# Kernel tuning notes

Measured on AMD Instinct MI355X. Metric: run time of the kernel, lower is better.

## Reference

```python
import jax, jax.numpy as jnp
import numpy as np

B, L, E, H = 1024, 18, 300, 300
VW, VS = 100000, 2186


def setup_inputs() -> dict:
    key = jax.random.key(0)
    ks = jax.random.split(key, 16)
    word = jax.random.randint(ks[0], (B, 1), 0, VW)
    sememes = jax.random.randint(ks[1], (B, L), 0, VS)
    word_table = jax.random.normal(ks[2], (VW, E), jnp.float32) * 0.1
    sem_table = jax.random.normal(ks[3], (VS, E), jnp.float32) * 0.1
    sem_table = sem_table.at[0].set(0.0)  # padding_idx=0 -> zero row
    s = 1.0 / np.sqrt(H)

    def u(k, shape):
        return jax.random.uniform(k, shape, jnp.float32, -s, s)

    return {
        "word": word, "sememes": sememes,
        "word_table": word_table, "sem_table": sem_table,
        "Wih_f": u(ks[4], (4 * H, 2 * E)), "Whh_f": u(ks[5], (4 * H, H)),
        "bih_f": u(ks[6], (4 * H,)), "bhh_f": u(ks[7], (4 * H,)),
        "Wih_b": u(ks[8], (4 * H, 2 * E)), "Whh_b": u(ks[9], (4 * H, H)),
        "bih_b": u(ks[10], (4 * H,)), "bhh_b": u(ks[11], (4 * H,)),
        "Wa": u(ks[12], (H, 2 * H)), "ba": jnp.zeros((H,), jnp.float32),
        "Wb": u(ks[13], (E, E)), "bb": jnp.zeros((E,), jnp.float32),
    }


def _lstm(x, Wih, Whh, bih, bhh, reverse):
    # x: [B, L, 2E]; PyTorch gate order i, f, g, o
    xg = jnp.einsum('ble,ge->blg', x, Wih) + bih + bhh  # [B, L, 4H]
    Hh = Whh.shape[1]
    Bn = x.shape[0]

    def step(carry, xt):
        h, c = carry
        g = xt + h @ Whh.T
        i, f, gg, o = jnp.split(g, 4, axis=-1)
        i = jax.nn.sigmoid(i)
        f = jax.nn.sigmoid(f)
        gg = jnp.tanh(gg)
        o = jax.nn.sigmoid(o)
        c = f * c + i * gg
        h = o * jnp.tanh(c)
        return (h, c), h

    init = (jnp.zeros((Bn, Hh), x.dtype), jnp.zeros((Bn, Hh), x.dtype))
    _, hs = jax.lax.scan(step, init, jnp.swapaxes(xg, 0, 1), reverse=reverse)
    return jnp.swapaxes(hs, 0, 1)  # [B, L, H]


def reference(word, sememes, word_table, sem_table,
              Wih_f, Whh_f, bih_f, bhh_f,
              Wih_b, Whh_b, bih_b, bhh_b,
              Wa, ba, Wb, bb):
    w = word_table[word[:, 0]]      # [B, E]
    s = sem_table[sememes]          # [B, L, E]
    # AvgPool2d((18,1)) over the L=18 axis (zeros included in the mean)
    a_g = jnp.mean(s, axis=1)       # [B, E]
    v_g = jax.nn.relu(a_g @ Wb.T + bb)  # dropout is identity at inference
    # Vectorized replacement of the per-element python loop:
    # padding slot (index 0 -> zero embedding) gets cat(sem, sem) = zeros,
    # otherwise cat(word_emb, sem).
    mask = (sememes == 0)[..., None]                    # [B, L, 1]
    first = jnp.where(mask, s, w[:, None, :])           # [B, L, E]
    x = jnp.concatenate([first, s], axis=-1)            # [B, L, 2E]
    hf = _lstm(x, Wih_f, Whh_f, bih_f, bhh_f, reverse=False)
    hb = _lstm(x, Wih_b, Whh_b, bih_b, bhh_b, reverse=True)
    Vh = jnp.concatenate([hf, hb], axis=-1)             # [B, L, 2H]
    V = jax.nn.relu(jnp.einsum('blh,oh->blo', Vh, Wa) + ba)
    return V, v_g
```

## Files before the change

### kernel.cpp

```cpp
#include <hip/hip_runtime.h>
#include <cstddef>
#include <cstdint>
#include <math.h>

#define B_   1024
#define L_   18
#define E_   300
#define H_   300
#define M_   (B_*L_)
#define G4_  (4*H_)
#define K2E_ (2*E_)

#define NPAD 2432
#define PSTR 2432
#define M2P  2304

#define OFF_P1   ((size_t)0)
#define OFF_P2   (OFF_P1 + (size_t)1024*PSTR)
#define OFF_HCAT (OFF_P2 + (size_t)M2P*PSTR)
#define OFF_AG   (OFF_HCAT + (size_t)M_*608/2)
#define OFF_WBT  (OFF_AG  + (size_t)B_*E_)
#define OFF_WFF  (OFF_WBT + 90000)
#define OFF_WFB  (OFF_WFF + 194560)
#define OFF_WAT  (OFF_WFB + 194560)
#define OFF_WCP  (OFF_WAT + 92416)
#define OFF_HP   (OFF_WCP + 778240)
#define OFF_C    (OFF_HP + 655360)

#define HPSTR 327680

#define VOFF ((size_t)M_*H_)

typedef short bf16x8 __attribute__((ext_vector_type(8)));
typedef float f32x4  __attribute__((ext_vector_type(4)));

__device__ __forceinline__ short f2bf(float f) {
    union { float f; uint32_t u; } c; c.f = f;
    uint32_t u = c.u + 0x7fffu + ((c.u >> 16) & 1u);
    return (short)(u >> 16);
}

__global__ void k_prep(const float* __restrict__ Wb, float* __restrict__ WbT)
{
    int idx = blockIdx.x * 256 + threadIdx.x;
    if (idx < 90000) {
        int o = idx % 300;
        int k = idx / 300;
        WbT[idx] = Wb[o * 300 + k];
    }
}

__global__ __launch_bounds__(256) void k_prep_wcp(const float* __restrict__ Wih_f,
                                                  const float* __restrict__ Wih_b,
                                                  short* __restrict__ WcatP)
{
    int idx = blockIdx.x * 256 + threadIdx.x;
    if (idx >= 2 * NPAD * 320) return;
    int p = idx / (NPAD * 320);
    int rem = idx - p * (NPAD * 320);
    int n = rem / 320;
    int kp = rem - n * 320;
    int fwd = (n < 1216);
    int nn = fwd ? n : n - 1216;
    float v = 0.f;
    if (kp < 300 && nn < G4_) {
        int u = nn >> 2, g = nn & 3;
        const float* W = fwd ? Wih_f : Wih_b;
        v = W[(size_t)(g * 300 + u) * K2E_ + (p ? 300 + kp : kp)];
    }
    WcatP[idx] = f2bf(v);
}

__global__ __launch_bounds__(256) void k_prep_whh(const float* __restrict__ Whh_f,
                                                  const float* __restrict__ Whh_b,
                                                  short* __restrict__ WFf,
                                                  short* __restrict__ WFb)
{
    int idx = blockIdx.x * 256 + threadIdx.x;
    if (idx >= 389120) return;
    int d = blockIdx.y;
    int chunk = idx >> 9;
    int rem   = idx & 511;
    int lane  = rem >> 3;
    int j     = rem & 7;
    int nt = chunk / 10, kt = chunk - nt * 10;
    int n = nt * 16 + (lane & 15);
    int k = kt * 32 + (lane >> 4) * 8 + j;
    float v = 0.f;
    if (n < G4_ && k < H_) {
        int u = n >> 2, g = n & 3;
        const float* W = d ? Whh_b : Whh_f;
        v = W[(size_t)(g * 300 + u) * H_ + k];
    }
    (d ? WFb : WFf)[idx] = f2bf(v);
}

__global__ __launch_bounds__(256) void k_prep_wa(const float* __restrict__ Wa,
                                                 short* __restrict__ WAT)
{
    int idx = blockIdx.x * 256 + threadIdx.x;
    if (idx >= 184832) return;
    int chunk = idx >> 9;
    int rem   = idx & 511;
    int lane  = rem >> 3;
    int j     = rem & 7;
    int nt = chunk / 19, kt = chunk - nt * 19;
    int o  = nt * 16 + (lane & 15);
    int kp = kt * 32 + (lane >> 4) * 8 + j;
    float v = 0.f;
    if (o < H_) {
        int k = -1;
        if (kp < 300)                   k = kp;
        else if (kp >= 304 && kp < 604) k = kp - 4;
        if (k >= 0) v = Wa[(size_t)o * K2E_ + k];
    }
    WAT[idx] = f2bf(v);
}

__global__ void k_zero(short* __restrict__ hcat, short* __restrict__ hp)
{
    int r = blockIdx.x * 256 + threadIdx.x;
    if (r < M_) {
        *(uint64_t*)&hcat[(size_t)r * 608 + 300] = 0ull;
        *(uint64_t*)&hcat[(size_t)r * 608 + 604] = 0ull;
    }
    uint64_t* hp8 = (uint64_t*)hp;
    for (int i = r; i < 327680; i += M_) hp8[i] = 0ull;
}

__global__ __launch_bounds__(256) void k_ag(const int* __restrict__ sem,
                                            const float* __restrict__ sem_table,
                                            float* __restrict__ ag)
{
    int b = blockIdx.x;
    __shared__ int sm[L_];
    if (threadIdx.x < L_) sm[threadIdx.x] = sem[b * L_ + threadIdx.x];
    __syncthreads();
    for (int e = threadIdx.x; e < E_; e += 256) {
        float s = 0.f;
        #pragma unroll
        for (int l = 0; l < L_; ++l) s += sem_table[sm[l] * E_ + e];
        ag[(size_t)b * E_ + e] = s * (1.0f / (float)L_);
    }
}

__global__ __launch_bounds__(256) void k_vg(const float* __restrict__ ag,
                                            const float* __restrict__ WbT,
                                            const float* __restrict__ bbv,
                                            float* __restrict__ out)
{
    int b0 = blockIdx.x * 16;
    __shared__ __align__(16) float ag_s[16 * E_];
    for (int idx = threadIdx.x; idx < 16 * E_; idx += 256)
        ag_s[idx] = ag[(size_t)b0 * E_ + idx];
    __syncthreads();
    for (int o = threadIdx.x; o < E_; o += 256) {
        float acc[16];
        #pragma unroll
        for (int i = 0; i < 16; ++i) acc[i] = 0.f;
        for (int k = 0; k < E_; ++k) {
            float w = WbT[k * E_ + o];
            #pragma unroll
            for (int i = 0; i < 16; ++i)
                acc[i] = fmaf(w, ag_s[i * E_ + k], acc[i]);
        }
        float bias = bbv[o];
        #pragma unroll
        for (int i = 0; i < 16; ++i) {
            float v = acc[i] + bias;
            out[VOFF + (size_t)(b0 + i) * E_ + o] = v > 0.f ? v : 0.f;
        }
    }
}

#define LDT 40

__global__ __launch_bounds__(256) void k_p(const int* __restrict__ word,
                                           const float* __restrict__ word_table,
                                           const float* __restrict__ sem_table,
                                           const short* __restrict__ WcatP,
                                           const float* __restrict__ bih_f,
                                           const float* __restrict__ bhh_f,
                                           const float* __restrict__ bih_b,
                                           const float* __restrict__ bhh_b,
                                           float* __restrict__ P1,
                                           float* __restrict__ P2)
{
    __shared__ __align__(16) short As[128 * LDT];
    __shared__ __align__(16) short Bs[128 * LDT];
    __shared__ const float* rowp[128];

    const int mb = blockIdx.x;
    const int p  = (mb >= 8);
    const int m0 = (p ? mb - 8 : mb) * 128;
    const int n0 = blockIdx.y * 128;
    const int tid = threadIdx.x;

    if (tid < 128) {
        int m = m0 + tid;
        rowp[tid] = p ? (m < 2186 ? sem_table + (size_t)m * E_ : (const float*)0)
                      : word_table + (size_t)word[m] * E_;
    }
    __syncthreads();

    f32x4 acc[4][4];
    #pragma unroll
    for (int i = 0; i < 4; ++i)
        #pragma unroll
        for (int j = 0; j < 4; ++j)
            acc[i][j] = (f32x4){0.f, 0.f, 0.f, 0.f};

    const int wv   = tid >> 6;
    const int lane = tid & 63;
    const int wm   = (wv >> 1) * 64;
    const int wn   = (wv & 1) * 64;
    const int lm   = lane & 15;
    const int quad = lane >> 4;

    const int r  = tid >> 1;
    const int kh = (tid & 1) * 16;
    const float* rp = rowp[r];
    const short* bsrc = WcatP + (size_t)p * (NPAD * 320) + (size_t)(n0 + r) * 320;

    for (int k0 = 0; k0 < 320; k0 += 32) {
        {
            const int kbase = k0 + kh;
            #pragma unroll
            for (int q = 0; q < 4; ++q) {
                int k = kbase + q * 4;
                float4 v = (k < E_ && rp) ? *(const float4*)&rp[k]
                                          : make_float4(0.f, 0.f, 0.f, 0.f);
                short4 s4;
                s4.x = f2bf(v.x); s4.y = f2bf(v.y);
                s4.z = f2bf(v.z); s4.w = f2bf(v.w);
                *(short4*)&As[r * LDT + kh + q * 4] = s4;
            }
        }
        {
            const short* src = bsrc + k0 + kh;
            *(int4*)&Bs[r * LDT + kh + 0] = *(const int4*)&src[0];
            *(int4*)&Bs[r * LDT + kh + 8] = *(const int4*)&src[8];
        }
        __syncthreads();

        bf16x8 af[4], bfr[4];
        #pragma unroll
        for (int i = 0; i < 4; ++i)
            af[i] = *(const bf16x8*)&As[(wm + 16 * i + lm) * LDT + quad * 8];
        #pragma unroll
        for (int j = 0; j < 4; ++j)
            bfr[j] = *(const bf16x8*)&Bs[(wn + 16 * j + lm) * LDT + quad * 8];
        #pragma unroll
        for (int i = 0; i < 4; ++i)
            #pragma unroll
            for (int j = 0; j < 4; ++j)
                acc[i][j] = __builtin_amdgcn_mfma_f32_16x16x32_bf16(
                    af[i], bfr[j], acc[i][j], 0, 0, 0);
        __syncthreads();
    }

    float* dst = p ? P2 : P1;
    #pragma unroll
    for (int j = 0; j < 4; ++j) {
        int n = n0 + wn + 16 * j + lm;
        float bias = 0.f;
        if (p) {
            int fwd = (n < 1216);
            int cc = fwd ? n : n - 1216;
            if (cc < G4_) {
                int u = cc >> 2, g = cc & 3;
                bias = fwd ? (bih_f[g * 300 + u] + bhh_f[g * 300 + u])
                           : (bih_b[g * 300 + u] + bhh_b[g * 300 + u]);
            }
        }
        #pragma unroll
        for (int i = 0; i < 4; ++i) {
            int mb2 = m0 + wm + 16 * i + quad * 4;
            #pragma unroll
            for (int reg = 0; reg < 4; ++reg)
                dst[(size_t)(mb2 + reg) * PSTR + n] = acc[i][j][reg] + bias;
        }
    }
}

__global__ __launch_bounds__(256) void k_step2(const float* __restrict__ P1,
                                               const float* __restrict__ P2,
                                               const int* __restrict__ sem,
                                               const short* __restrict__ WFf,
                                               const short* __restrict__ WFb,
                                               short* __restrict__ hp,
                                               float* __restrict__ cbuf,
                                               short* __restrict__ hcat,
                                               int s)
{
    const int d  = blockIdx.z;
    const short* WF = d ? WFb : WFf;
    const int t = d ? (L_ - 1 - s) : s;
    const short* hin = hp + (size_t)(d * 2 + ((s + 1) & 1)) * HPSTR;
    short*      hout = hp + (size_t)(d * 2 + (s & 1)) * HPSTR;
    short* hc = hcat + (d ? 304 : 0);
    float* cp = cbuf + (size_t)d * (1024 * 304);

    const int m0 = blockIdx.x * 64;
    const int rt0 = blockIdx.x * 4;
    const int nb = blockIdx.y;
    const int tid  = threadIdx.x;
    const int lane = tid & 63;
    const int wv   = tid >> 6;
    const int lm   = lane & 15;
    const int quad = lane >> 4;

    __shared__ __align__(16) float Cs[64][68];

    f32x4 acc[4];
    #pragma unroll
    for (int mt = 0; mt < 4; ++mt) acc[mt] = (f32x4){0.f, 0.f, 0.f, 0.f};

    if (s > 0) {
        const short* wp = WF + ((size_t)(nb * 4 + wv) * 10) * 512 + lane * 8;
        #pragma unroll
        for (int kt = 0; kt < 10; ++kt) {
            bf16x8 bf = *(const bf16x8*)(wp + kt * 512);
            #pragma unroll
            for (int mt = 0; mt < 4; ++mt) {
                bf16x8 af = *(const bf16x8*)&hin[((size_t)(rt0 + mt) * 10 + kt) * 512 + lane * 8];
                acc[mt] = __builtin_amdgcn_mfma_f32_16x16x32_bf16(af, bf, acc[mt], 0, 0, 0);
            }
        }
    }

    #pragma unroll
    for (int mt = 0; mt < 4; ++mt)
        #pragma unroll
        for (int r = 0; r < 4; ++r)
            Cs[mt * 16 + quad * 4 + r][wv * 16 + lm] = acc[mt][r];
    __syncthreads();

    const int m = tid >> 2;
    const int q = tid & 3;
    const int b = m0 + m;
    const int u0 = nb * 16 + 4 * q;
    if (u0 < H_) {
        const int svt = sem[b * L_ + t];
        const size_t pcol = (size_t)d * 1216 + 4 * u0;
        const float* p2r = P2 + (size_t)svt * PSTR + pcol;
        const float* p1r = P1 + (size_t)b * PSTR + pcol;
        float4 xv[4];
        #pragma unroll
        for (int i = 0; i < 4; ++i) xv[i] = *(const float4*)&p2r[4 * i];
        if (svt != 0) {
            #pragma unroll
            for (int i = 0; i < 4; ++i) {
                float4 a = *(const float4*)&p1r[4 * i];
                xv[i].x += a.x; xv[i].y += a.y; xv[i].z += a.z; xv[i].w += a.w;
            }
        }
        float4 cpv = (s > 0) ? *(const float4*)&cp[(size_t)b * 304 + u0]
                             : make_float4(0.f, 0.f, 0.f, 0.f);
        float cold[4] = {cpv.x, cpv.y, cpv.z, cpv.w};
        float cnew[4];
        short hn[4];
        #pragma unroll
        for (int i = 0; i < 4; ++i) {
            float4 gv = *(const float4*)&Cs[m][16 * q + 4 * i];
            float gi = xv[i].x + gv.x;
            float gf = xv[i].y + gv.y;
            float gg = xv[i].z + gv.z;
            float go = xv[i].w + gv.w;
            float iv = 1.f / (1.f + __expf(-gi));
            float fv = 1.f / (1.f + __expf(-gf));
            float tg = 1.f - 2.f / (__expf(2.f * gg) + 1.f);
            float ov = 1.f / (1.f + __expf(-go));
            float cc = fmaf(fv, cold[i], iv * tg);
            cnew[i] = cc;
            float th = 1.f - 2.f / (__expf(2.f * cc) + 1.f);
            hn[i] = f2bf(ov * th);
        }
        *(float4*)&cp[(size_t)b * 304 + u0] = make_float4(cnew[0], cnew[1], cnew[2], cnew[3]);
        short4 h4 = {hn[0], hn[1], hn[2], hn[3]};
        {
            int rt = b >> 4, ktu = u0 >> 5;
            int fl = (b & 15) | (((u0 >> 3) & 3) << 4);
            *(short4*)&hout[((size_t)(rt * 10 + ktu) * 512) + fl * 8 + (u0 & 7)] = h4;
        }
        *(short4*)&hc[((size_t)b * L_ + t) * 608 + u0] = h4;
    }
}

__global__ __launch_bounds__(256) void k_out(const short* __restrict__ hcat,
                                             const short* __restrict__ WAT,
                                             const float* __restrict__ ba,
                                             float* __restrict__ out)
{
    const int m0 = blockIdx.x * 64;
    const int tid = threadIdx.x;
    const int lane = tid & 63;
    const int wv = tid >> 6;
    const int lm = lane & 15;
    const int quad = lane >> 4;

    __shared__ __align__(16) short A_s[64][616];

    for (int idx = tid; idx < 4864; idx += 256) {
        int r = idx / 76, c8 = idx - r * 76;
        *(int4*)&A_s[r][c8 * 8] = *(const int4*)&hcat[(size_t)(m0 + r) * 608 + c8 * 8];
    }
    __syncthreads();

    f32x4 acc[4][5];
    #pragma unroll
    for (int mt = 0; mt < 4; ++mt)
        #pragma unroll
        for (int q = 0; q < 5; ++q)
            acc[mt][q] = (f32x4){0.f, 0.f, 0.f, 0.f};

    for (int kt = 0; kt < 19; ++kt) {
        bf16x8 af[4];
        #pragma unroll
        for (int mt = 0; mt < 4; ++mt)
            af[mt] = *(const bf16x8*)&A_s[mt * 16 + lm][kt * 32 + quad * 8];
        #pragma unroll
        for (int q = 0; q < 5; ++q) {
            int nt = wv + 4 * q;
            if (nt < 19) {
                bf16x8 bf = *(const bf16x8*)&WAT[((size_t)(nt * 19 + kt) * 64 + lane) * 8];
                #pragma unroll
                for (int mt = 0; mt < 4; ++mt)
                    acc[mt][q] = __builtin_amdgcn_mfma_f32_16x16x32_bf16(
                        af[mt], bf, acc[mt][q], 0, 0, 0);
            }
        }
    }

    #pragma unroll
    for (int q = 0; q < 5; ++q) {
        int nt = wv + 4 * q;
        if (nt < 19) {
            int o = nt * 16 + lm;
            if (o < H_) {
                float bias = ba[o];
                #pragma unroll
                for (int mt = 0; mt < 4; ++mt) {
                    #pragma unroll
                    for (int r = 0; r < 4; ++r) {
                        int m = m0 + mt * 16 + quad * 4 + r;
                        float v = acc[mt][q][r] + bias;
                        out[(size_t)m * H_ + o] = v > 0.f ? v : 0.f;
                    }
                }
            }
        }
    }
}

extern "C" void kernel_launch(void* const* d_in, const int* in_sizes, int n_in,
                              void* d_out, int out_size, void* d_ws, size_t ws_size,
                              hipStream_t stream) {
    const int*   word       = (const int*)  d_in[0];
    const int*   sem        = (const int*)  d_in[1];
    const float* word_table = (const float*)d_in[2];
    const float* sem_table  = (const float*)d_in[3];
    const float* Wih_f      = (const float*)d_in[4];
    const float* Whh_f      = (const float*)d_in[5];
    const float* bih_f      = (const float*)d_in[6];
    const float* bhh_f      = (const float*)d_in[7];
    const float* Wih_b      = (const float*)d_in[8];
    const float* Whh_b      = (const float*)d_in[9];
    const float* bih_b      = (const float*)d_in[10];
    const float* bhh_b      = (const float*)d_in[11];
    const float* Wa         = (const float*)d_in[12];
    const float* ba         = (const float*)d_in[13];
    const float* Wb         = (const float*)d_in[14];
    const float* bbv        = (const float*)d_in[15];

    float* out = (float*)d_out;
    float* ws  = (float*)d_ws;

    float* P1    = ws + OFF_P1;
    float* P2    = ws + OFF_P2;
    short* hcat  = (short*)(ws + OFF_HCAT);
    float* ag    = ws + OFF_AG;
    float* WbT   = ws + OFF_WBT;
    short* WFf   = (short*)(ws + OFF_WFF);
    short* WFb   = (short*)(ws + OFF_WFB);
    short* WAT   = (short*)(ws + OFF_WAT);
    short* WcatP = (short*)(ws + OFF_WCP);
    short* hp    = (short*)(ws + OFF_HP);
    float* cbuf  = ws + OFF_C;

    k_prep<<<dim3(352), dim3(256), 0, stream>>>(Wb, WbT);
    k_prep_wcp<<<dim3((2 * NPAD * 320 + 255) / 256), dim3(256), 0, stream>>>(
        Wih_f, Wih_b, WcatP);
    k_prep_whh<<<dim3(1520, 2), dim3(256), 0, stream>>>(Whh_f, Whh_b, WFf, WFb);
    k_prep_wa<<<dim3(722), dim3(256), 0, stream>>>(Wa, WAT);
    k_zero<<<dim3((M_ + 255) / 256), dim3(256), 0, stream>>>(hcat, hp);

    k_ag<<<dim3(B_), dim3(256), 0, stream>>>(sem, sem_table, ag);
    k_vg<<<dim3(B_ / 16), dim3(256), 0, stream>>>(ag, WbT, bbv, out);

    k_p<<<dim3(26, 19), dim3(256), 0, stream>>>(
        word, word_table, sem_table, WcatP,
        bih_f, bhh_f, bih_b, bhh_b, P1, P2);

    for (int s = 0; s < L_; ++s) {
        k_step2<<<dim3(16, 19, 2), dim3(256), 0, stream>>>(
            P1, P2, sem, WFf, WFb, hp, cbuf, hcat, s);
    }

    k_out<<<dim3(M_ / 64), dim3(256), 0, stream>>>(hcat, WAT, ba, out);
}
```

Baseline: 533.2 us.

## Fuse LSTM recurrence into one persistent cooperative kernel with grid sync

The 18 per-timestep k_step2 launches are replaced by one cooperative kernel, k_rec2, that loops over all timesteps and uses a grid-wide sync between steps. Each block keeps its slice of the recurrent weights and its cell state in registers and handles 128 rows instead of 64, which removes per-step launch overhead and repeated weight and cell-state traffic. In exchange, grid syncs and heavier register use per block limit it to 2 blocks per CU, and the old per-step path stays as a fallback when cooperative launch is unavailable. The k_zero kernel is also dropped, so the padding columns of hcat are no longer zeroed; k_out could then pick up NaN garbage from the workspace even though the matching weights are zero.

```diff
diff --git a/kernel.cpp b/kernel.cpp
--- a/kernel.cpp
+++ b/kernel.cpp
@@ -1,7 +1,10 @@
 #include <hip/hip_runtime.h>
+#include <hip/hip_cooperative_groups.h>
 #include <cstddef>
 #include <cstdint>
 #include <math.h>
+
+namespace cg = cooperative_groups;
 
 #define B_   1024
 #define L_   18
@@ -117,17 +120,6 @@
     WAT[idx] = f2bf(v);
 }
 
-__global__ void k_zero(short* __restrict__ hcat, short* __restrict__ hp)
-{
-    int r = blockIdx.x * 256 + threadIdx.x;
-    if (r < M_) {
-        *(uint64_t*)&hcat[(size_t)r * 608 + 300] = 0ull;
-        *(uint64_t*)&hcat[(size_t)r * 608 + 604] = 0ull;
-    }
-    uint64_t* hp8 = (uint64_t*)hp;
-    for (int i = r; i < 327680; i += M_) hp8[i] = 0ull;
-}
-
 __global__ __launch_bounds__(256) void k_ag(const int* __restrict__ sem,
                                             const float* __restrict__ sem_table,
                                             float* __restrict__ ag)
@@ -283,6 +275,129 @@
     }
 }
 
+__global__ __launch_bounds__(256, 2) void k_rec2(const float* __restrict__ P1,
+                                                 const float* __restrict__ P2,
+                                                 const int* __restrict__ sem,
+                                                 const short* __restrict__ WFf,
+                                                 const short* __restrict__ WFb,
+                                                 short* __restrict__ hp,
+                                                 short* __restrict__ hcat)
+{
+    cg::grid_group gg = cg::this_grid();
+
+    const int d  = blockIdx.z;
+    const short* WF = d ? WFb : WFf;
+    short* hc = hcat + (d ? 304 : 0);
+    const int rt0 = blockIdx.x * 8;
+    const int nb  = blockIdx.y;
+    const int tid  = threadIdx.x;
+    const int lane = tid & 63;
+    const int wv   = tid >> 6;
+    const int quad = lane >> 4;
+
+    __shared__ __align__(16) float Cs[128][68];
+
+    bf16x8 bfr[10];
+    {
+        const short* wp = WF + ((size_t)(nb * 4 + wv) * 10) * 512 + lane * 8;
+        #pragma unroll
+        for (int kt = 0; kt < 10; ++kt)
+            bfr[kt] = *(const bf16x8*)(wp + kt * 512);
+    }
+
+    const int m  = tid >> 1;
+    const int q  = tid & 1;
+    const int b  = rt0 * 16 + m;
+    const int u0 = nb * 16 + 8 * q;
+    const bool a0 = (u0 < H_);
+    const bool a1 = (u0 + 4 < H_);
+    const size_t pcol = (size_t)d * 1216 + 4 * u0;
+    const float* p1r = P1 + (size_t)b * PSTR + pcol;
+    float c8[8] = {0.f,0.f,0.f,0.f,0.f,0.f,0.f,0.f};
+
+    size_t hofs;
+    {
+        int rt = b >> 4, ktu = u0 >> 5;
+        int fl = (b & 15) | (((u0 >> 3) & 3) << 4);
+        hofs = ((size_t)(rt * 10 + ktu) * 512) + (size_t)fl * 8 + (u0 & 7);
+    }
+
+    for (int s = 0; s < L_; ++s) {
+        const int t = d ? (L_ - 1 - s) : s;
+        const short* hin = hp + (size_t)(d * 2 + ((s + 1) & 1)) * HPSTR;
+        short*      hout = hp + (size_t)(d * 2 + (s & 1)) * HPSTR;
+
+        float4 xv[8];
+        {
+            const int svt = sem[b * L_ + t];
+            const float* p2r = P2 + (size_t)svt * PSTR + pcol;
+            #pragma unroll
+            for (int i = 0; i < 8; ++i) xv[i] = *(const float4*)&p2r[4 * i];
+            if (svt != 0) {
+                #pragma unroll
+                for (int i = 0; i < 8; ++i) {
+                    float4 a = *(const float4*)&p1r[4 * i];
+                    xv[i].x += a.x; xv[i].y += a.y; xv[i].z += a.z; xv[i].w += a.w;
+                }
+            }
+        }
+
+        f32x4 acc[8];
+        #pragma unroll
+        for (int mt = 0; mt < 8; ++mt) acc[mt] = (f32x4){0.f, 0.f, 0.f, 0.f};
+        if (s > 0) {
+            #pragma unroll
+            for (int kt = 0; kt < 10; ++kt) {
+                #pragma unroll
+                for (int mt = 0; mt < 8; ++mt) {
+                    bf16x8 af = *(const bf16x8*)&hin[((size_t)(rt0 + mt) * 10 + kt) * 512 + lane * 8];
+                    acc[mt] = __builtin_amdgcn_mfma_f32_16x16x32_bf16(af, bfr[kt], acc[mt], 0, 0, 0);
+                }
+            }
+        }
+
+        #pragma unroll
+        for (int mt = 0; mt < 8; ++mt)
+            #pragma unroll
+            for (int r = 0; r < 4; ++r)
+                Cs[mt * 16 + quad * 4 + r][wv * 16 + (lane & 15)] = acc[mt][r];
+        __syncthreads();
+
+        {
+            short hn[8];
+            #pragma unroll
+            for (int i = 0; i < 8; ++i) {
+                float4 gv = *(const float4*)&Cs[m][32 * q + 4 * i];
+                float gi = xv[i].x + gv.x;
+                float gf = xv[i].y + gv.y;
+                float gg2 = xv[i].z + gv.z;
+                float go = xv[i].w + gv.w;
+                float iv = 1.f / (1.f + __expf(-gi));
+                float fv = 1.f / (1.f + __expf(-gf));
+                float tg = 1.f - 2.f / (__expf(2.f * gg2) + 1.f);
+                float ov = 1.f / (1.f + __expf(-go));
+                float cc = fmaf(fv, c8[i], iv * tg);
+                c8[i] = cc;
+                float th = 1.f - 2.f / (__expf(2.f * cc) + 1.f);
+                hn[i] = f2bf(ov * th);
+            }
+            if (a0) {
+                short4 h4 = {hn[0], hn[1], hn[2], hn[3]};
+                *(short4*)&hout[hofs] = h4;
+                *(short4*)&hc[((size_t)b * L_ + t) * 608 + u0] = h4;
+            }
+            if (a1) {
+                short4 h4 = {hn[4], hn[5], hn[6], hn[7]};
+                *(short4*)&hout[hofs + 4] = h4;
+                *(short4*)&hc[((size_t)b * L_ + t) * 608 + u0 + 4] = h4;
+            }
+        }
+
+        __threadfence();
+        gg.sync();
+    }
+}
+
 __global__ __launch_bounds__(256) void k_step2(const float* __restrict__ P1,
                                                const float* __restrict__ P2,
                                                const int* __restrict__ sem,
@@ -307,7 +422,6 @@
     const int tid  = threadIdx.x;
     const int lane = tid & 63;
     const int wv   = tid >> 6;
-    const int lm   = lane & 15;
     const int quad = lane >> 4;
 
     __shared__ __align__(16) float Cs[64][68];
@@ -333,7 +447,7 @@
     for (int mt = 0; mt < 4; ++mt)
         #pragma unroll
         for (int r = 0; r < 4; ++r)
-            Cs[mt * 16 + quad * 4 + r][wv * 16 + lm] = acc[mt][r];
+            Cs[mt * 16 + quad * 4 + r][wv * 16 + (lane & 15)] = acc[mt][r];
     __syncthreads();
 
     const int m = tid >> 2;
@@ -381,7 +495,7 @@
         {
             int rt = b >> 4, ktu = u0 >> 5;
             int fl = (b & 15) | (((u0 >> 3) & 3) << 4);
-            *(short4*)&hout[((size_t)(rt * 10 + ktu) * 512) + fl * 8 + (u0 & 7)] = h4;
+            *(short4*)&hout[((size_t)(rt * 10 + ktu) * 512) + (size_t)fl * 8 + (u0 & 7)] = h4;
         }
         *(short4*)&hc[((size_t)b * L_ + t) * 608 + u0] = h4;
     }
@@ -493,7 +607,6 @@
         Wih_f, Wih_b, WcatP);
     k_prep_whh<<<dim3(1520, 2), dim3(256), 0, stream>>>(Whh_f, Whh_b, WFf, WFb);
     k_prep_wa<<<dim3(722), dim3(256), 0, stream>>>(Wa, WAT);
-    k_zero<<<dim3((M_ + 255) / 256), dim3(256), 0, stream>>>(hcat, hp);
 
     k_ag<<<dim3(B_), dim3(256), 0, stream>>>(sem, sem_table, ag);
     k_vg<<<dim3(B_ / 16), dim3(256), 0, stream>>>(ag, WbT, bbv, out);
@@ -502,9 +615,28 @@
         word, word_table, sem_table, WcatP,
         bih_f, bhh_f, bih_b, bhh_b, P1, P2);
 
-    for (int s = 0; s < L_; ++s) {
-        k_step2<<<dim3(16, 19, 2), dim3(256), 0, stream>>>(
-            P1, P2, sem, WFf, WFb, hp, cbuf, hcat, s);
+    int useCoop = 0;
+    {
+        int dev = 0, coopAttr = 0, numCU = 0, maxBlk = 0;
+        (void)hipGetDevice(&dev);
+        (void)hipDeviceGetAttribute(&coopAttr, hipDeviceAttributeCooperativeLaunch, dev);
+        (void)hipDeviceGetAttribute(&numCU, hipDeviceAttributeMultiprocessorCount, dev);
+        (void)hipOccupancyMaxActiveBlocksPerMultiprocessor(&maxBlk, k_rec2, 256, 0);
+        if (coopAttr && (long)maxBlk * (long)numCU >= 304) useCoop = 1;
+    }
+    if (useCoop) {
+        void* args[] = {(void*)&P1, (void*)&P2, (void*)&sem,
+                        (void*)&WFf, (void*)&WFb, (void*)&hp, (void*)&hcat};
+        hipError_t e = hipLaunchCooperativeKernel((const void*)k_rec2,
+                                                  dim3(8, 19, 2), dim3(256),
+                                                  args, 0, stream);
+        if (e != hipSuccess) useCoop = 0;
+    }
+    if (!useCoop) {
+        for (int s = 0; s < L_; ++s) {
+            k_step2<<<dim3(16, 19, 2), dim3(256), 0, stream>>>(
+                P1, P2, sem, WFf, WFb, hp, cbuf, hcat, s);
+        }
     }
 
     k_out<<<dim3(M_ / 64), dim3(256), 0, stream>>>(hcat, WAT, ba, out);
```

Measured after the change: 532.2 us. About the same (-0.2%).
